# Kernel optimization log

Hardware: AMD Instinct MI355X
Metric: run time of the kernel (lower is better)

The kernel has to match this reference:

```python
import jax, jax.numpy as jnp
import numpy as np

B, L = 512, 200
WORD_V, PATH_V = 100000, 200000
E, D = 128, 384


def setup_inputs() -> dict:
    key = jax.random.key(0)
    ks = jax.random.split(key, 10)
    inp = {
        "x_s1": jax.random.randint(ks[0], (B, L), 0, WORD_V),
        "path1": jax.random.randint(ks[1], (B, L), 0, PATH_V),
        "x_t1": jax.random.randint(ks[2], (B, L), 0, WORD_V),
        "x_s2": jax.random.randint(ks[3], (B, L), 0, WORD_V),
        "path2": jax.random.randint(ks[4], (B, L), 0, PATH_V),
        "x_t2": jax.random.randint(ks[5], (B, L), 0, WORD_V),
        # learned parameters
        "word_emb": jax.random.normal(ks[6], (WORD_V, E), dtype=jnp.float32) * 0.02,
        "path_emb": jax.random.normal(ks[7], (PATH_V, E), dtype=jnp.float32) * 0.02,
        "W_fc": jax.random.normal(ks[8], (D, 3 * E), dtype=jnp.float32) * (1.0 / np.sqrt(3 * E)),  # nn.Linear weight [out, in], no bias
        "attn": jax.random.uniform(ks[9], (D, 1), dtype=jnp.float32),
    }
    return inp


def _extract(xs, path, xt, word_emb, path_emb, W_fc, attn):
    # gather + concat -> [B, L, 3E]
    ctx = jnp.concatenate([word_emb[xs], path_emb[path], word_emb[xt]], axis=-1)
    # linear (no bias, dropout is identity at eval) + tanh -> [B, L, D]
    h = jnp.tanh(jnp.einsum('blf,df->bld', ctx, W_fc))
    # attention scores [B, L, 1]; the zeros mask in the original is a no-op
    scores = jnp.einsum('bld,do->blo', h, attn)
    a = jax.nn.softmax(scores, axis=1)
    code_vec = jnp.sum(h * a, axis=1)  # [B, D]
    return code_vec, a


def reference(x_s1, path1, x_t1, x_s2, path2, x_t2, word_emb, path_emb, W_fc, attn):
    cv1, _ = _extract(x_s1, path1, x_t1, word_emb, path_emb, W_fc, attn)
    cv2, _ = _extract(x_s2, path2, x_t2, word_emb, path_emb, W_fc, attn)
    return (cv1, cv2)
```

## Files before the change

### kernel.cpp

```cpp
#include <hip/hip_runtime.h>
#include <hip/hip_bf16.h>

#define B_N 512
#define L_N 200
#define E_N 128
#define K_N 384
#define D_N 384

typedef __bf16 v8bf  __attribute__((ext_vector_type(8)));
typedef float  v4f   __attribute__((ext_vector_type(4)));
typedef unsigned int v4u __attribute__((ext_vector_type(4)));
typedef unsigned short v8us __attribute__((ext_vector_type(8)));

__device__ __forceinline__ unsigned short f2bf(float f) {
    union { __bf16 b; unsigned short u; } cv;
    cv.b = (__bf16)f;
    return cv.u;
}
__device__ __forceinline__ float fast_tanh(float x) {
    float e = __expf(2.f * x);
    return 1.f - 2.f * __builtin_amdgcn_rcpf(e + 1.f);
}

__global__ void pack_w(const float* __restrict__ W, unsigned short* __restrict__ Wp) {
    int gid  = blockIdx.x * 256 + threadIdx.x;
    int lane = gid & 63;
    int u    = gid >> 6;
    int gn   = u % 24;
    int kk   = u / 24;
    int c    = lane & 15, quad = lane >> 4;
    const float* src = W + (gn * 16 + c) * K_N + kk * 32 + quad * 8;
    ushort4 lo, hi;
    lo.x = f2bf(src[0]); lo.y = f2bf(src[1]); lo.z = f2bf(src[2]); lo.w = f2bf(src[3]);
    hi.x = f2bf(src[4]); hi.y = f2bf(src[5]); hi.z = f2bf(src[6]); hi.w = f2bf(src[7]);
    ushort4* dst = (ushort4*)(Wp + (size_t)gid * 8);
    dst[0] = lo; dst[1] = hi;
}

#define SEG_E 8192

template<int MT>
__device__ __forceinline__ void compute_chunk(
    const unsigned short* Alds, const v4u* wp4, float (*sp)[64],
    int wv, int lane, int quad, int c,
    float an0, float an1, float an2,
    v4f (&acc)[4][3])
{
    const int arow = c * 128;
    const int akey = (c & 7) << 3;
    const int q8   = quad * 8;

    #pragma unroll 2
    for (int kk = 0; kk < 12; ++kk) {
        v8bf b0 = __builtin_bit_cast(v8bf, wp4[(kk * 24 + wv * 3 + 0) * 64 + lane]);
        v8bf b1 = __builtin_bit_cast(v8bf, wp4[(kk * 24 + wv * 3 + 1) * 64 + lane]);
        v8bf b2 = __builtin_bit_cast(v8bf, wp4[(kk * 24 + wv * 3 + 2) * 64 + lane]);
        const int soff = (((kk & 3) * 32 + q8) ^ akey);
        #pragma unroll
        for (int mt = 0; mt < MT; ++mt) {
            v8bf a = *(const v8bf*)&Alds[(kk >> 2) * SEG_E + mt * 2048 + arow + soff];
            acc[mt][0] = __builtin_amdgcn_mfma_f32_16x16x32_bf16(a, b0, acc[mt][0], 0, 0, 0);
            acc[mt][1] = __builtin_amdgcn_mfma_f32_16x16x32_bf16(a, b1, acc[mt][1], 0, 0, 0);
            acc[mt][2] = __builtin_amdgcn_mfma_f32_16x16x32_bf16(a, b2, acc[mt][2], 0, 0, 0);
        }
    }
    #pragma unroll
    for (int mt = 0; mt < MT; ++mt) {
        #pragma unroll
        for (int r = 0; r < 4; ++r) {
            float h0 = fast_tanh(acc[mt][0][r]);
            float h1 = fast_tanh(acc[mt][1][r]);
            float h2 = fast_tanh(acc[mt][2][r]);
            acc[mt][0][r] = h0; acc[mt][1][r] = h1; acc[mt][2][r] = h2;
            float sv = h0 * an0 + h1 * an1 + h2 * an2;
            sv += __shfl_xor(sv, 1);
            sv += __shfl_xor(sv, 2);
            sv += __shfl_xor(sv, 4);
            sv += __shfl_xor(sv, 8);
            if (c == 0) sp[wv][mt * 16 + quad * 4 + r] = sv;
        }
    }
}

__global__ __launch_bounds__(512, 4)
void c2v_fused(const int* __restrict__ xs1, const int* __restrict__ ph1,
               const int* __restrict__ xt1,
               const int* __restrict__ xs2, const int* __restrict__ ph2,
               const int* __restrict__ xt2,
               const float* __restrict__ wemb, const float* __restrict__ pemb,
               const unsigned short* __restrict__ Wp,
               const float* __restrict__ attn,
               float* __restrict__ out)
{
    const int tid  = threadIdx.x;
    const int wv   = tid >> 6;
    const int lane = tid & 63;
    const int quad = lane >> 4;
    const int c    = lane & 15;
    const int b    = blockIdx.x;
    const int pass = blockIdx.y;

    const int* xs = pass ? xs2 : xs1;
    const int* ph = pass ? ph2 : ph1;
    const int* xt = pass ? xt2 : xt1;

    __shared__ __align__(16) unsigned short Alds[3 * SEG_E];
    __shared__ float sp[8][64];
    __shared__ int   ilds[3 * 208];

    for (int u = tid; u < 624; u += 512) {
        int s = u / 208, g = u - s * 208;
        const int* tab = (s == 0) ? xs : (s == 1) ? ph : xt;
        ilds[u] = (g < L_N) ? tab[b * L_N + g] : 0;
    }

    const float an0 = attn[(wv * 3 + 0) * 16 + c];
    const float an1 = attn[(wv * 3 + 1) * 16 + c];
    const float an2 = attn[(wv * 3 + 2) * 16 + c];

    float o0 = 0.f, o1 = 0.f, o2 = 0.f;
    float Mrun = -1e30f, Zrun = 0.f;

    const v4u* wp4 = (const v4u*)Wp;

    __syncthreads();

    for (int chunk = 0; chunk < 4; ++chunk) {
        const int row0  = chunk * 64;
        const int mrows = (chunk == 3) ? 16 : 64;
        const int mtmax = (chunk == 3) ? 1 : 4;

        float4 fa[6], fb[6];
        #pragma unroll
        for (int i = 0; i < 6; ++i) {
            int u = i * 512 + tid;
            int s = u >> 10;
            int rr = u & 1023;
            int m = rr >> 4;
            int j = rr & 15;
            int g = row0 + m;
            if (m < mrows && g < L_N) {
                const float* eb = (s == 1) ? pemb : wemb;
                const float* src = eb + (size_t)ilds[s * 208 + g] * E_N + j * 8;
                fa[i] = *(const float4*)src;
                fb[i] = *(const float4*)(src + 4);
            } else {
                fa[i].x = fa[i].y = fa[i].z = fa[i].w = 0.f;
                fb[i] = fa[i];
            }
        }
        v8us cv[6];
        #pragma unroll
        for (int i = 0; i < 6; ++i) {
            cv[i][0] = f2bf(fa[i].x); cv[i][1] = f2bf(fa[i].y);
            cv[i][2] = f2bf(fa[i].z); cv[i][3] = f2bf(fa[i].w);
            cv[i][4] = f2bf(fb[i].x); cv[i][5] = f2bf(fb[i].y);
            cv[i][6] = f2bf(fb[i].z); cv[i][7] = f2bf(fb[i].w);
        }

        __syncthreads();

        #pragma unroll
        for (int i = 0; i < 6; ++i) {
            int u = i * 512 + tid;
            int s = u >> 10, rr = u & 1023, m = rr >> 4, j = rr & 15;
            if (m < mrows)
                *(v8us*)&Alds[s * SEG_E + m * 128 + ((j * 8) ^ ((m & 7) << 3))] = cv[i];
        }
        __syncthreads();

        v4f acc[4][3];
        #pragma unroll
        for (int i = 0; i < 4; ++i)
            #pragma unroll
            for (int j = 0; j < 3; ++j)
                acc[i][j] = (v4f){0.f, 0.f, 0.f, 0.f};

        if (chunk < 3)
            compute_chunk<4>(Alds, wp4, sp, wv, lane, quad, c, an0, an1, an2, acc);
        else
            compute_chunk<1>(Alds, wp4, sp, wv, lane, quad, c, an0, an1, an2, acc);
        __syncthreads();

        {
            int g = row0 + lane;
            float s = sp[0][lane] + sp[1][lane] + sp[2][lane] + sp[3][lane]
                    + sp[4][lane] + sp[5][lane] + sp[6][lane] + sp[7][lane];
            if (g >= L_N) s = -1e30f;
            float mx = s;
            #pragma unroll
            for (int off = 32; off > 0; off >>= 1) mx = fmaxf(mx, __shfl_xor(mx, off));
            float Mnew  = fmaxf(Mrun, mx);
            float alpha = __expf(Mrun - Mnew);
            float e = (g < L_N) ? __expf(s - Mnew) : 0.f;
            float zc = e;
            #pragma unroll
            for (int off = 32; off > 0; off >>= 1) zc += __shfl_xor(zc, off);
            Zrun = Zrun * alpha + zc;
            Mrun = Mnew;

            float p0 = 0.f, p1 = 0.f, p2 = 0.f;
            #pragma unroll
            for (int mt = 0; mt < 4; ++mt) {
                if (mt < mtmax) {
                    #pragma unroll
                    for (int r = 0; r < 4; ++r) {
                        float w = __shfl(e, mt * 16 + quad * 4 + r);
                        p0 += w * acc[mt][0][r];
                        p1 += w * acc[mt][1][r];
                        p2 += w * acc[mt][2][r];
                    }
                }
            }
            o0 = o0 * alpha + p0;
            o1 = o1 * alpha + p1;
            o2 = o2 * alpha + p2;
        }
    }

    const float zinv = __builtin_amdgcn_rcpf(Zrun);

    float* outp = out + (size_t)(pass * B_N + b) * D_N;
    o0 += __shfl_xor(o0, 16); o0 += __shfl_xor(o0, 32);
    o1 += __shfl_xor(o1, 16); o1 += __shfl_xor(o1, 32);
    o2 += __shfl_xor(o2, 16); o2 += __shfl_xor(o2, 32);
    if (quad == 0) {
        outp[(wv * 3 + 0) * 16 + c] = o0 * zinv;
        outp[(wv * 3 + 1) * 16 + c] = o1 * zinv;
        outp[(wv * 3 + 2) * 16 + c] = o2 * zinv;
    }
}

extern "C" void kernel_launch(void* const* d_in, const int* in_sizes, int n_in,
                              void* d_out, int out_size, void* d_ws, size_t ws_size,
                              hipStream_t stream) {
    unsigned short* Wp = (unsigned short*)d_ws;
    pack_w<<<72, 256, 0, stream>>>((const float*)d_in[8], Wp);
    dim3 grid(B_N, 2, 1);
    c2v_fused<<<grid, 512, 0, stream>>>(
        (const int*)d_in[0], (const int*)d_in[1], (const int*)d_in[2],
        (const int*)d_in[3], (const int*)d_in[4], (const int*)d_in[5],
        (const float*)d_in[6], (const float*)d_in[7],
        Wp, (const float*)d_in[9],
        (float*)d_out);
}
```

Baseline: 288.2 us.

## Prefetch next chunk's embedding gathers during MFMA and tanh phase

Splits the per-chunk work so the global embedding gathers for the next 64-row chunk are issued after the current chunk's MFMAs and before the tanh/score step, then stored to LDS after the barrier. The aim is to hide gather latency behind compute within a single block. In exchange, fa/fb prefetch registers stay live across compute, so the launch bound is relaxed from 4 to 2 blocks per SM, which may lower occupancy.

```diff
diff --git a/kernel.cpp b/kernel.cpp
--- a/kernel.cpp
+++ b/kernel.cpp
@@ -40,11 +40,9 @@
 #define SEG_E 8192
 
 template<int MT>
-__device__ __forceinline__ void compute_chunk(
-    const unsigned short* Alds, const v4u* wp4, float (*sp)[64],
-    int wv, int lane, int quad, int c,
-    float an0, float an1, float an2,
-    v4f (&acc)[4][3])
+__device__ __forceinline__ void mfma_chunk(
+    const unsigned short* Alds, const v4u* wp4,
+    int wv, int lane, int quad, int c, v4f (&acc)[4][3])
 {
     const int arow = c * 128;
     const int akey = (c & 7) << 3;
@@ -64,6 +62,13 @@
             acc[mt][2] = __builtin_amdgcn_mfma_f32_16x16x32_bf16(a, b2, acc[mt][2], 0, 0, 0);
         }
     }
+}
+
+template<int MT>
+__device__ __forceinline__ void tanh_score(
+    float (*sp)[64], int wv, int quad, int c,
+    float an0, float an1, float an2, v4f (&acc)[4][3])
+{
     #pragma unroll
     for (int mt = 0; mt < MT; ++mt) {
         #pragma unroll
@@ -82,7 +87,7 @@
     }
 }
 
-__global__ __launch_bounds__(512, 4)
+__global__ __launch_bounds__(512, 2)
 void c2v_fused(const int* __restrict__ xs1, const int* __restrict__ ph1,
                const int* __restrict__ xt1,
                const int* __restrict__ xs2, const int* __restrict__ ph2,
@@ -123,14 +128,11 @@
 
     const v4u* wp4 = (const v4u*)Wp;
 
-    __syncthreads();
-
-    for (int chunk = 0; chunk < 4; ++chunk) {
-        const int row0  = chunk * 64;
-        const int mrows = (chunk == 3) ? 16 : 64;
-        const int mtmax = (chunk == 3) ? 1 : 4;
-
-        float4 fa[6], fb[6];
+    float4 fa[6], fb[6];
+
+    auto load_units = [&](int nc) {
+        const int r0 = nc * 64;
+        const int mr = (nc == 3) ? 16 : 64;
         #pragma unroll
         for (int i = 0; i < 6; ++i) {
             int u = i * 512 + tid;
@@ -138,8 +140,8 @@
             int rr = u & 1023;
             int m = rr >> 4;
             int j = rr & 15;
-            int g = row0 + m;
-            if (m < mrows && g < L_N) {
+            int g = r0 + m;
+            if (m < mr && g < L_N) {
                 const float* eb = (s == 1) ? pemb : wemb;
                 const float* src = eb + (size_t)ilds[s * 208 + g] * E_N + j * 8;
                 fa[i] = *(const float4*)src;
@@ -149,25 +151,32 @@
                 fb[i] = fa[i];
             }
         }
-        v8us cv[6];
-        #pragma unroll
-        for (int i = 0; i < 6; ++i) {
-            cv[i][0] = f2bf(fa[i].x); cv[i][1] = f2bf(fa[i].y);
-            cv[i][2] = f2bf(fa[i].z); cv[i][3] = f2bf(fa[i].w);
-            cv[i][4] = f2bf(fb[i].x); cv[i][5] = f2bf(fb[i].y);
-            cv[i][6] = f2bf(fb[i].z); cv[i][7] = f2bf(fb[i].w);
-        }
-
-        __syncthreads();
-
+    };
+
+    auto store_units = [&](int nc) {
+        const int mr = (nc == 3) ? 16 : 64;
         #pragma unroll
         for (int i = 0; i < 6; ++i) {
             int u = i * 512 + tid;
             int s = u >> 10, rr = u & 1023, m = rr >> 4, j = rr & 15;
-            if (m < mrows)
-                *(v8us*)&Alds[s * SEG_E + m * 128 + ((j * 8) ^ ((m & 7) << 3))] = cv[i];
-        }
-        __syncthreads();
+            v8us t;
+            t[0] = f2bf(fa[i].x); t[1] = f2bf(fa[i].y);
+            t[2] = f2bf(fa[i].z); t[3] = f2bf(fa[i].w);
+            t[4] = f2bf(fb[i].x); t[5] = f2bf(fb[i].y);
+            t[6] = f2bf(fb[i].z); t[7] = f2bf(fb[i].w);
+            if (m < mr)
+                *(v8us*)&Alds[s * SEG_E + m * 128 + ((j * 8) ^ ((m & 7) << 3))] = t;
+        }
+    };
+
+    __syncthreads();
+    load_units(0);
+    store_units(0);
+    __syncthreads();
+
+    for (int chunk = 0; chunk < 4; ++chunk) {
+        const int row0  = chunk * 64;
+        const int mtmax = (chunk == 3) ? 1 : 4;
 
         v4f acc[4][3];
         #pragma unroll
@@ -176,11 +185,17 @@
             for (int j = 0; j < 3; ++j)
                 acc[i][j] = (v4f){0.f, 0.f, 0.f, 0.f};
 
-        if (chunk < 3)
-            compute_chunk<4>(Alds, wp4, sp, wv, lane, quad, c, an0, an1, an2, acc);
-        else
-            compute_chunk<1>(Alds, wp4, sp, wv, lane, quad, c, an0, an1, an2, acc);
+        if (chunk < 3) {
+            mfma_chunk<4>(Alds, wp4, wv, lane, quad, c, acc);
+            load_units(chunk + 1);
+            tanh_score<4>(sp, wv, quad, c, an0, an1, an2, acc);
+        } else {
+            mfma_chunk<1>(Alds, wp4, wv, lane, quad, c, acc);
+            tanh_score<1>(sp, wv, quad, c, an0, an1, an2, acc);
+        }
         __syncthreads();
+
+        if (chunk < 3) store_units(chunk + 1);
 
         {
             int g = row0 + lane;
@@ -216,6 +231,8 @@
             o1 = o1 * alpha + p1;
             o2 = o2 * alpha + p2;
         }
+
+        if (chunk < 3) __syncthreads();
     }
 
     const float zinv = __builtin_amdgcn_rcpf(Zrun);
```

Measured after the change: 389.8 us. 35.2% more time.

## Shrink row chunk from 64 to 32 to halve LDS and register footprint

Applied to the files above, without the earlier changes.

The fused gather-GEMM-attention kernel now processes the 200 path-contexts in seven chunks of 32 rows instead of four chunks of 64. The A-tile LDS buffer, score scratch and accumulator arrays are each halved, and each thread gathers one row-segment per stream per chunk. The intent is to cut LDS and register pressure so more blocks fit per CU and gather latency overlaps better. The cost is more chunk iterations, each with its own barriers and online-softmax update, and the packed weight fragments are reloaded from global memory roughly twice as often.

```diff
diff --git a/kernel.cpp b/kernel.cpp
--- a/kernel.cpp
+++ b/kernel.cpp
@@ -37,14 +37,12 @@
     dst[0] = lo; dst[1] = hi;
 }
 
-#define SEG_E 8192
+#define SEG_E 4096
 
 template<int MT>
-__device__ __forceinline__ void compute_chunk(
-    const unsigned short* Alds, const v4u* wp4, float (*sp)[64],
-    int wv, int lane, int quad, int c,
-    float an0, float an1, float an2,
-    v4f (&acc)[4][3])
+__device__ __forceinline__ void mfma_chunk(
+    const unsigned short* Alds, const v4u* wp4,
+    int wv, int lane, int quad, int c, v4f (&acc)[2][3])
 {
     const int arow = c * 128;
     const int akey = (c & 7) << 3;
@@ -64,6 +62,13 @@
             acc[mt][2] = __builtin_amdgcn_mfma_f32_16x16x32_bf16(a, b2, acc[mt][2], 0, 0, 0);
         }
     }
+}
+
+template<int MT>
+__device__ __forceinline__ void tanh_score(
+    float (*sp)[32], int wv, int quad, int c,
+    float an0, float an1, float an2, v4f (&acc)[2][3])
+{
     #pragma unroll
     for (int mt = 0; mt < MT; ++mt) {
         #pragma unroll
@@ -105,7 +110,7 @@
     const int* xt = pass ? xt2 : xt1;
 
     __shared__ __align__(16) unsigned short Alds[3 * SEG_E];
-    __shared__ float sp[8][64];
+    __shared__ float sp[8][32];
     __shared__ int   ilds[3 * 208];
 
     for (int u = tid; u < 624; u += 512) {
@@ -123,76 +128,80 @@
 
     const v4u* wp4 = (const v4u*)Wp;
 
+    const int sm = tid >> 4;
+    const int sj = tid & 15;
+
     __syncthreads();
 
-    for (int chunk = 0; chunk < 4; ++chunk) {
-        const int row0  = chunk * 64;
-        const int mrows = (chunk == 3) ? 16 : 64;
-        const int mtmax = (chunk == 3) ? 1 : 4;
-
-        float4 fa[6], fb[6];
-        #pragma unroll
-        for (int i = 0; i < 6; ++i) {
-            int u = i * 512 + tid;
-            int s = u >> 10;
-            int rr = u & 1023;
-            int m = rr >> 4;
-            int j = rr & 15;
-            int g = row0 + m;
-            if (m < mrows && g < L_N) {
+    for (int chunk = 0; chunk < 7; ++chunk) {
+        const int row0  = chunk * 32;
+        const int mrows = (chunk == 6) ? 16 : 32;
+        const int mtmax = (chunk == 6) ? 1 : 2;
+
+        const int  sg  = row0 + sm;
+        const bool act = (sm < mrows) && (sg < L_N);
+        float4 fa[3], fb[3];
+        #pragma unroll
+        for (int s = 0; s < 3; ++s) {
+            if (act) {
                 const float* eb = (s == 1) ? pemb : wemb;
-                const float* src = eb + (size_t)ilds[s * 208 + g] * E_N + j * 8;
-                fa[i] = *(const float4*)src;
-                fb[i] = *(const float4*)(src + 4);
+                const float* src = eb + (size_t)ilds[s * 208 + sg] * E_N + sj * 8;
+                fa[s] = *(const float4*)src;
+                fb[s] = *(const float4*)(src + 4);
             } else {
-                fa[i].x = fa[i].y = fa[i].z = fa[i].w = 0.f;
-                fb[i] = fa[i];
+                fa[s].x = fa[s].y = fa[s].z = fa[s].w = 0.f;
+                fb[s] = fa[s];
             }
         }
-        v8us cv[6];
-        #pragma unroll
-        for (int i = 0; i < 6; ++i) {
-            cv[i][0] = f2bf(fa[i].x); cv[i][1] = f2bf(fa[i].y);
-            cv[i][2] = f2bf(fa[i].z); cv[i][3] = f2bf(fa[i].w);
-            cv[i][4] = f2bf(fb[i].x); cv[i][5] = f2bf(fb[i].y);
-            cv[i][6] = f2bf(fb[i].z); cv[i][7] = f2bf(fb[i].w);
+        v8us cv[3];
+        #pragma unroll
+        for (int s = 0; s < 3; ++s) {
+            cv[s][0] = f2bf(fa[s].x); cv[s][1] = f2bf(fa[s].y);
+            cv[s][2] = f2bf(fa[s].z); cv[s][3] = f2bf(fa[s].w);
+            cv[s][4] = f2bf(fb[s].x); cv[s][5] = f2bf(fb[s].y);
+            cv[s][6] = f2bf(fb[s].z); cv[s][7] = f2bf(fb[s].w);
         }
 
         __syncthreads();
 
-        #pragma unroll
-        for (int i = 0; i < 6; ++i) {
-            int u = i * 512 + tid;
-            int s = u >> 10, rr = u & 1023, m = rr >> 4, j = rr & 15;
-            if (m < mrows)
-                *(v8us*)&Alds[s * SEG_E + m * 128 + ((j * 8) ^ ((m & 7) << 3))] = cv[i];
+        if (sm < mrows) {
+            const int soff = sm * 128 + ((sj * 8) ^ ((sm & 7) << 3));
+            #pragma unroll
+            for (int s = 0; s < 3; ++s)
+                *(v8us*)&Alds[s * SEG_E + soff] = cv[s];
         }
         __syncthreads();
 
-        v4f acc[4][3];
-        #pragma unroll
-        for (int i = 0; i < 4; ++i)
+        v4f acc[2][3];
+        #pragma unroll
+        for (int i = 0; i < 2; ++i)
             #pragma unroll
             for (int j = 0; j < 3; ++j)
                 acc[i][j] = (v4f){0.f, 0.f, 0.f, 0.f};
 
-        if (chunk < 3)
-            compute_chunk<4>(Alds, wp4, sp, wv, lane, quad, c, an0, an1, an2, acc);
-        else
-            compute_chunk<1>(Alds, wp4, sp, wv, lane, quad, c, an0, an1, an2, acc);
+        if (chunk < 6) {
+            mfma_chunk<2>(Alds, wp4, wv, lane, quad, c, acc);
+            tanh_score<2>(sp, wv, quad, c, an0, an1, an2, acc);
+        } else {
+            mfma_chunk<1>(Alds, wp4, wv, lane, quad, c, acc);
+            tanh_score<1>(sp, wv, quad, c, an0, an1, an2, acc);
+        }
         __syncthreads();
 
         {
             int g = row0 + lane;
-            float s = sp[0][lane] + sp[1][lane] + sp[2][lane] + sp[3][lane]
-                    + sp[4][lane] + sp[5][lane] + sp[6][lane] + sp[7][lane];
-            if (g >= L_N) s = -1e30f;
+            float s = -1e30f;
+            if (lane < 32) {
+                float t = sp[0][lane] + sp[1][lane] + sp[2][lane] + sp[3][lane]
+                        + sp[4][lane] + sp[5][lane] + sp[6][lane] + sp[7][lane];
+                if (g < L_N) s = t;
+            }
             float mx = s;
             #pragma unroll
             for (int off = 32; off > 0; off >>= 1) mx = fmaxf(mx, __shfl_xor(mx, off));
             float Mnew  = fmaxf(Mrun, mx);
             float alpha = __expf(Mrun - Mnew);
-            float e = (g < L_N) ? __expf(s - Mnew) : 0.f;
+            float e = (lane < 32 && g < L_N) ? __expf(s - Mnew) : 0.f;
             float zc = e;
             #pragma unroll
             for (int off = 32; off > 0; off >>= 1) zc += __shfl_xor(zc, off);
@@ -201,7 +210,7 @@
 
             float p0 = 0.f, p1 = 0.f, p2 = 0.f;
             #pragma unroll
-            for (int mt = 0; mt < 4; ++mt) {
+            for (int mt = 0; mt < 2; ++mt) {
                 if (mt < mtmax) {
                     #pragma unroll
                     for (int r = 0; r < 4; ++r) {
```

Result: slower. 306.6 us (+6.4%).
